# Optimization experiments

Hardware: AMD Instinct MI355X
Metric: run time of the kernel (lower is better)

## Reference

```python
import jax, jax.numpy as jnp
import numpy as np

N_NODES = 100000
N_EDGES = 1600000


def _gcn_conv(h, W, b, src, dst, n):
    """PyG GCNConv: linear, add self-loops, sym-normalized scatter-add, bias."""
    h = h @ W  # [n, out]
    # degree with self-loops: 1 (self loop) + in-degree over dst
    deg = jnp.ones((n,), dtype=h.dtype).at[dst].add(1.0)
    dinv = jax.lax.rsqrt(deg)  # deg >= 1, safe
    norm = dinv[src] * dinv[dst]  # [E]
    out = jnp.zeros_like(h).at[dst].add(norm[:, None] * h[src])
    out = out + (dinv * dinv)[:, None] * h  # self-loop contribution
    return out + b


def setup_inputs() -> dict:
    key = jax.random.key(0)
    ks = jax.random.split(key, 6)
    x = jax.random.normal(ks[0], (N_NODES, 5), dtype=jnp.float32)
    edge_index = jax.random.randint(ks[1], (2, N_EDGES), 0, N_NODES, dtype=jnp.int64)
    aff_w = jax.random.normal(ks[2], (3, 1), dtype=jnp.float32)
    cog_w = jax.random.normal(ks[3], (2, 1), dtype=jnp.float32)
    W1 = jax.random.normal(ks[4], (5, 64), dtype=jnp.float32) * 0.5
    b1 = jnp.zeros((64,), dtype=jnp.float32)
    W2 = jax.random.normal(ks[5], (64, 2), dtype=jnp.float32) * 0.125
    b2 = jnp.zeros((2,), dtype=jnp.float32)
    return {"x": x, "edge_index": edge_index, "aff_w": aff_w, "cog_w": cog_w,
            "W1": W1, "b1": b1, "W2": W2, "b2": b2}


def reference(x, edge_index, aff_w, cog_w, W1, b1, W2, b2):
    src, dst = edge_index[0], edge_index[1]
    n = x.shape[0]
    aff = x[:, :3]  # affective_indices = [0,1,2]
    cog = x[:, 3:5]  # cognitive_indices = [3,4]
    # attention: scores are [n,1]; softmax over dim=1 (size-1 axis), faithful to source
    s_a = jax.nn.softmax(aff @ aff_w, axis=1)
    s_c = jax.nn.softmax(cog @ cog_w, axis=1)
    h = jnp.concatenate([aff * s_a, cog * s_c], axis=1)  # [n,5]
    h = _gcn_conv(h, W1, b1, src, dst, n)
    h = jax.nn.relu(h)  # dropout is identity in eval mode
    h = _gcn_conv(h, W2, b2, src, dst, n)
    return jax.nn.log_softmax(h, axis=1)
```

## Files before the change

kernel.cpp:

```cpp
#include <hip/hip_runtime.h>


#define NPB     256
#define BSHIFT  8
#define BINCAP  6144
#define MAXBINS 512
#define ABLK    512
#define APT     8
#define BBLK    512
#define ROUNDS  3

__global__ __launch_bounds__(ABLK) void binA_k(const int* __restrict__ src, const int* __restrict__ dst,
                                               int E, int nbins, int* __restrict__ cursor,
                                               unsigned int* __restrict__ bpk) {
    __shared__ int hist[MAXBINS];
    __shared__ int gbase[MAXBINS];
    int t = threadIdx.x;
    hist[t] = 0;
    __syncthreads();
    int base = blockIdx.x * (ABLK * APT);
    int s_[APT], d_[APT], r_[APT];
#pragma unroll
    for (int r = 0; r < APT / 4; ++r) {
        int j0 = base + (r * ABLK + t) * 4;
        if (j0 + 3 < E) {
            int4 s4 = *(const int4*)(src + j0);
            int4 d4 = *(const int4*)(dst + j0);
            s_[r * 4 + 0] = s4.x; s_[r * 4 + 1] = s4.y; s_[r * 4 + 2] = s4.z; s_[r * 4 + 3] = s4.w;
            d_[r * 4 + 0] = d4.x; d_[r * 4 + 1] = d4.y; d_[r * 4 + 2] = d4.z; d_[r * 4 + 3] = d4.w;
#pragma unroll
            for (int q = 0; q < 4; ++q)
                r_[r * 4 + q] = atomicAdd(&hist[d_[r * 4 + q] >> BSHIFT], 1);
        } else {
#pragma unroll
            for (int q = 0; q < 4; ++q) {
                int e = j0 + q;
                if (e < E) {
                    s_[r * 4 + q] = src[e]; d_[r * 4 + q] = dst[e];
                    r_[r * 4 + q] = atomicAdd(&hist[d_[r * 4 + q] >> BSHIFT], 1);
                } else d_[r * 4 + q] = -1;
            }
        }
    }
    __syncthreads();
    if (t < nbins) {
        int h = hist[t];
        gbase[t] = h ? atomicAdd(&cursor[t], h) : 0;
    }
    __syncthreads();
#pragma unroll
    for (int q = 0; q < APT; ++q) {
        if (d_[q] >= 0) {
            int b = d_[q] >> BSHIFT;
            int pos = gbase[b] + r_[q];
            if (pos < BINCAP)
                bpk[(size_t)b * BINCAP + pos] = ((unsigned int)s_[q] << 8) | (unsigned int)(d_[q] & (NPB - 1));
        }
    }
}

__global__ __launch_bounds__(BBLK) void build_k(const int* __restrict__ cursor,
                                                const unsigned int* __restrict__ bpk,
                                                const float* __restrict__ x,
                                                int* __restrict__ sorted,
                                                int* __restrict__ row_start,
                                                unsigned short* __restrict__ row_cnt,
                                                float* __restrict__ dinv, float* __restrict__ y8, int n) {
    __shared__ int cnt[NPB];
    __shared__ int offs[NPB];
    __shared__ int srt[BINCAP];
    __shared__ int wsum[4];
    int b = blockIdx.x, t = threadIdx.x;
    if (t < NPB) cnt[t] = 0;
    __syncthreads();
    int m = cursor[b]; if (m > BINCAP) m = BINCAP;
    const unsigned int* pk = bpk + (size_t)b * BINCAP;

    unsigned int pv[ROUNDS][4];
    int rk[ROUNDS][4];
#pragma unroll
    for (int q = 0; q < ROUNDS; ++q) {
        int j0 = q * (BBLK * 4) + t * 4;
        if (j0 + 3 < m) {
            uint4 v = *(const uint4*)(pk + j0);
            pv[q][0] = v.x; pv[q][1] = v.y; pv[q][2] = v.z; pv[q][3] = v.w;
            rk[q][0] = atomicAdd(&cnt[v.x & 255u], 1);
            rk[q][1] = atomicAdd(&cnt[v.y & 255u], 1);
            rk[q][2] = atomicAdd(&cnt[v.z & 255u], 1);
            rk[q][3] = atomicAdd(&cnt[v.w & 255u], 1);
        } else {
#pragma unroll
            for (int qq = 0; qq < 4; ++qq) {
                int j = j0 + qq;
                if (j < m) { pv[q][qq] = pk[j]; rk[q][qq] = atomicAdd(&cnt[pv[q][qq] & 255u], 1); }
                else pv[q][qq] = 0xffffffffu;
            }
        }
    }
    __syncthreads();
    int c_ = 0, v = 0;
    int lane = t & 63, w = t >> 6;
    if (t < NPB) {
        c_ = cnt[t];
        v = c_;
#pragma unroll
        for (int dlt = 1; dlt < 64; dlt <<= 1) {
            int u = __shfl_up(v, dlt, 64);
            if (lane >= dlt) v += u;
        }
        if (lane == 63) wsum[w] = v;
    }
    __syncthreads();
    if (t < NPB) {
        int wo = 0;
#pragma unroll
        for (int k = 0; k < 4; ++k) if (k < w) wo += wsum[k];
        offs[t] = wo + v - c_;
    }
    __syncthreads();
#pragma unroll
    for (int q = 0; q < ROUNDS; ++q) {
#pragma unroll
        for (int qq = 0; qq < 4; ++qq) {
            unsigned int p = pv[q][qq];
            if (p != 0xffffffffu) {
                int j0 = q * (BBLK * 4) + t * 4 + qq;
                if (j0 < m) srt[offs[p & 255u] + rk[q][qq]] = (int)(p >> 8);
            }
        }
    }
    __syncthreads();
    int gb = b * BINCAP;
    for (int j0 = t * 4; j0 + 3 < m; j0 += BBLK * 4)
        *(int4*)(sorted + gb + j0) = *(const int4*)(srt + j0);
    if (t < 4) {
        int start = m & ~3;
        int j = start + t;
        if (j < m) sorted[gb + j] = srt[j];
    }
    int i = b * NPB + t;
    if (t < NPB && i < n) {
        row_start[i] = gb + offs[t];
        row_cnt[i] = (unsigned short)c_;
        float di = rsqrtf(1.0f + (float)c_);
        dinv[i] = di;
#pragma unroll
        for (int k = 0; k < 5; ++k) y8[(size_t)i * 8 + k] = di * x[i * 5 + k];
    }
}

__global__ __launch_bounds__(256) void gath1_mlp_k(const int* __restrict__ sorted,
                                                   const int* __restrict__ row_start,
                                                   const unsigned short* __restrict__ row_cnt,
                                                   const float* __restrict__ y8,
                                                   const float* __restrict__ dinv,
                                                   const float* __restrict__ W1, const float* __restrict__ b1,
                                                   const float* __restrict__ W2,
                                                   float* __restrict__ gy, int n) {
    __shared__ float W1s[320], b1s[64], W2s[128];
    int t = threadIdx.x;
    { int j = t; if (j < 320) W1s[j] = W1[j]; j = t + 256; if (j < 320) W1s[j] = W1[j]; }
    if (t < 64) b1s[t] = b1[t];
    if (t >= 64 && t < 192) W2s[t - 64] = W2[t - 64];
    __syncthreads();
    int grp = t >> 2, lane = t & 3;
    int i = blockIdx.x * 64 + grp;
    if (i >= n) return;
    int st = row_start[i];
    int e  = st + row_cnt[i];
    float a0 = 0.f, a1 = 0.f, a2 = 0.f, a3 = 0.f, a4 = 0.f;
    for (int j = st + lane; j < e; j += 4) {
        int s = sorted[j];
        float4 A = *(const float4*)(y8 + (size_t)s * 8);
        a0 += A.x; a1 += A.y; a2 += A.z; a3 += A.w;
        a4 += y8[(size_t)s * 8 + 4];
    }
    a0 += __shfl_xor(a0, 1); a0 += __shfl_xor(a0, 2);
    a1 += __shfl_xor(a1, 1); a1 += __shfl_xor(a1, 2);
    a2 += __shfl_xor(a2, 1); a2 += __shfl_xor(a2, 2);
    a3 += __shfl_xor(a3, 1); a3 += __shfl_xor(a3, 2);
    a4 += __shfl_xor(a4, 1); a4 += __shfl_xor(a4, 2);
    float4 S = *(const float4*)(y8 + (size_t)i * 8);
    float s4 = y8[(size_t)i * 8 + 4];
    float di = dinv[i];
    float v0 = di * (a0 + S.x);
    float v1 = di * (a1 + S.y);
    float v2 = di * (a2 + S.z);
    float v3 = di * (a3 + S.w);
    float v4 = di * (a4 + s4);
    float g0 = 0.f, g1 = 0.f;
#pragma unroll
    for (int q = 0; q < 16; ++q) {
        int jj = lane + q * 4;
        float h = b1s[jj];
        h = fmaf(v0, W1s[0 * 64 + jj], h);
        h = fmaf(v1, W1s[1 * 64 + jj], h);
        h = fmaf(v2, W1s[2 * 64 + jj], h);
        h = fmaf(v3, W1s[3 * 64 + jj], h);
        h = fmaf(v4, W1s[4 * 64 + jj], h);
        h = fmaxf(h, 0.f);
        g0 = fmaf(h, W2s[2 * jj], g0);
        g1 = fmaf(h, W2s[2 * jj + 1], g1);
    }
    g0 += __shfl_xor(g0, 1); g0 += __shfl_xor(g0, 2);
    g1 += __shfl_xor(g1, 1); g1 += __shfl_xor(g1, 2);
    if (lane == 0) {
        gy[i * 2] = di * g0; gy[i * 2 + 1] = di * g1;
    }
}

__global__ __launch_bounds__(256) void gath2_final_k(const int* __restrict__ sorted,
                                                     const int* __restrict__ row_start,
                                                     const unsigned short* __restrict__ row_cnt,
                                                     const float* __restrict__ gy,
                                                     const float* __restrict__ dinv,
                                                     const float* __restrict__ b2,
                                                     float* __restrict__ out, int n) {
    int t = threadIdx.x;
    int grp = t >> 2, lane = t & 3;
    int i = blockIdx.x * 64 + grp;
    if (i >= n) return;
    int st = row_start[i];
    int e  = st + row_cnt[i];
    float t0 = 0.f, t1 = 0.f;
    for (int j = st + lane; j < e; j += 4) {
        int s = sorted[j];
        float2 v = *(const float2*)(gy + (size_t)s * 2);
        t0 += v.x; t1 += v.y;
    }
    t0 += __shfl_xor(t0, 1); t0 += __shfl_xor(t0, 2);
    t1 += __shfl_xor(t1, 1); t1 += __shfl_xor(t1, 2);
    if (lane == 0) {
        float2 Sg = *(const float2*)(gy + (size_t)i * 2);
        float di = dinv[i];
        float o0 = di * (t0 + Sg.x) + b2[0];
        float o1 = di * (t1 + Sg.y) + b2[1];
        float mx = fmaxf(o0, o1);
        float lse = mx + logf(expf(o0 - mx) + expf(o1 - mx));
        out[i * 2]     = o0 - lse;
        out[i * 2 + 1] = o1 - lse;
    }
}

#define CAP 48
__global__ void fill_k(const int* __restrict__ src, const int* __restrict__ dst,
                       int E, int n, int* __restrict__ cnt, int* __restrict__ bucket) {
    int e = blockIdx.x * blockDim.x + threadIdx.x;
    if (e >= E) return;
    int s = src[e], d = dst[e];
    int slot = atomicAdd(&cnt[d], 1);
    if (slot < CAP) bucket[slot * n + d] = s;
}
__global__ void dinv_y_k(const float* __restrict__ x, const int* __restrict__ cnt,
                         float* __restrict__ dinv, float* __restrict__ y, int n) {
    int i = blockIdx.x * blockDim.x + threadIdx.x;
    if (i >= n) return;
    float di = rsqrtf(1.0f + (float)cnt[i]);
    dinv[i] = di;
#pragma unroll
    for (int k = 0; k < 5; ++k) y[i * 5 + k] = di * x[i * 5 + k];
}
__global__ void gather1_mlp_k(const float* __restrict__ x, const float* __restrict__ y,
                              const float* __restrict__ dinv, const int* __restrict__ cnt,
                              const int* __restrict__ bucket, int n,
                              const float* __restrict__ W1, const float* __restrict__ b1,
                              const float* __restrict__ W2,
                              float* __restrict__ g, float* __restrict__ gy) {
    __shared__ float W1s[320]; __shared__ float b1s[64]; __shared__ float W2s[128];
    int t = threadIdx.x;
    for (int j = t; j < 320; j += blockDim.x) W1s[j] = W1[j];
    if (t < 64) { b1s[t] = b1[t]; W2s[2 * t] = W2[2 * t]; W2s[2 * t + 1] = W2[2 * t + 1]; }
    __syncthreads();
    int i = blockIdx.x * blockDim.x + t;
    if (i >= n) return;
    int c = cnt[i]; if (c > CAP) c = CAP;
    float a0 = 0, a1 = 0, a2 = 0, a3 = 0, a4 = 0;
    for (int j = 0; j < c; ++j) {
        int s = bucket[j * n + i];
        const float* ys = y + s * 5;
        a0 += ys[0]; a1 += ys[1]; a2 += ys[2]; a3 += ys[3]; a4 += ys[4];
    }
    float di = dinv[i], d2 = di * di;
    float v0 = di * a0 + d2 * x[i * 5 + 0], v1 = di * a1 + d2 * x[i * 5 + 1];
    float v2 = di * a2 + d2 * x[i * 5 + 2], v3 = di * a3 + d2 * x[i * 5 + 3];
    float v4 = di * a4 + d2 * x[i * 5 + 4];
    float g0 = 0.f, g1 = 0.f;
#pragma unroll
    for (int j = 0; j < 64; ++j) {
        float h = b1s[j];
        h = fmaf(v0, W1s[j], h); h = fmaf(v1, W1s[64 + j], h); h = fmaf(v2, W1s[128 + j], h);
        h = fmaf(v3, W1s[192 + j], h); h = fmaf(v4, W1s[256 + j], h);
        h = fmaxf(h, 0.f);
        g0 = fmaf(h, W2s[2 * j], g0); g1 = fmaf(h, W2s[2 * j + 1], g1);
    }
    g[i * 2] = g0; g[i * 2 + 1] = g1;
    gy[i * 2] = di * g0; gy[i * 2 + 1] = di * g1;
}
__global__ void gather2_final_fb_k(const float* __restrict__ g, const float* __restrict__ gy,
                                   const float* __restrict__ dinv, const int* __restrict__ cnt,
                                   const int* __restrict__ bucket, int n,
                                   const float* __restrict__ b2, float* __restrict__ out) {
    int i = blockIdx.x * blockDim.x + threadIdx.x;
    if (i >= n) return;
    int c = cnt[i]; if (c > CAP) c = CAP;
    float t0 = 0.f, t1 = 0.f;
    for (int j = 0; j < c; ++j) {
        int s = bucket[j * n + i];
        t0 += gy[s * 2]; t1 += gy[s * 2 + 1];
    }
    float di = dinv[i], d2 = di * di;
    float o0 = di * t0 + d2 * g[i * 2] + b2[0];
    float o1 = di * t1 + d2 * g[i * 2 + 1] + b2[1];
    float mx = fmaxf(o0, o1);
    float lse = mx + logf(expf(o0 - mx) + expf(o1 - mx));
    out[i * 2] = o0 - lse; out[i * 2 + 1] = o1 - lse;
}

extern "C" void kernel_launch(void* const* d_in, const int* in_sizes, int n_in,
                              void* d_out, int out_size, void* d_ws, size_t ws_size,
                              hipStream_t stream) {
    const float* x  = (const float*)d_in[0];
    const int*   ei = (const int*)d_in[1];
    const float* W1 = (const float*)d_in[4];
    const float* b1 = (const float*)d_in[5];
    const float* W2 = (const float*)d_in[6];
    const float* b2 = (const float*)d_in[7];
    float* out = (float*)d_out;

    const int n = in_sizes[0] / 5;
    const int E = in_sizes[1] / 2;
    const int* src = ei;
    const int* dst = ei + E;

    const int nbins = (n + NPB - 1) >> BSHIFT;
    size_t need = (size_t)MAXBINS * 4 + (size_t)nbins * BINCAP * 8 +
                  (size_t)n * (4 + 2 + 4 + 32 + 8) + 64;

    if (nbins <= MAXBINS && n < (1 << 24) && ws_size >= need) {
        int* cursor = (int*)d_ws;
        unsigned int* bpk = (unsigned int*)(cursor + MAXBINS);
        int* sorted = (int*)(bpk + (size_t)nbins * BINCAP);
        int* row_start = sorted + (size_t)nbins * BINCAP;
        unsigned short* row_cnt = (unsigned short*)(row_start + n);
        float* dinv = (float*)(row_cnt + ((n + 1) & ~1));
        float* y8 = dinv + n;
        float* gy = y8 + 8 * (size_t)n;

        hipMemsetAsync(cursor, 0, MAXBINS * sizeof(int), stream);
        int ablocks = (E + ABLK * APT - 1) / (ABLK * APT);
        binA_k<<<ablocks, ABLK, 0, stream>>>(src, dst, E, nbins, cursor, bpk);
        build_k<<<nbins, BBLK, 0, stream>>>(cursor, bpk, x, sorted, row_start, row_cnt, dinv, y8, n);
        int g64 = (n + 63) / 64;
        gath1_mlp_k<<<g64, 256, 0, stream>>>(sorted, row_start, row_cnt, y8, dinv, W1, b1, W2, gy, n);
        gath2_final_k<<<g64, 256, 0, stream>>>(sorted, row_start, row_cnt, gy, dinv, b2, out, n);
    } else {
        const int BLK = 256;
        const int ngrid = (n + BLK - 1) / BLK;
        const int egrid = (E + BLK - 1) / BLK;
        int*   cnt    = (int*)d_ws;
        int*   bucket = cnt + n;
        float* dinv   = (float*)(bucket + (size_t)CAP * n);
        float* y      = dinv + n;
        float* g      = y + 5 * (size_t)n;
        float* gy     = g + 2 * (size_t)n;
        hipMemsetAsync(cnt, 0, (size_t)n * sizeof(int), stream);
        fill_k<<<egrid, BLK, 0, stream>>>(src, dst, E, n, cnt, bucket);
        dinv_y_k<<<ngrid, BLK, 0, stream>>>(x, cnt, dinv, y, n);
        gather1_mlp_k<<<ngrid, BLK, 0, stream>>>(x, y, dinv, cnt, bucket, n, W1, b1, W2, g, gy);
        gather2_final_fb_k<<<ngrid, BLK, 0, stream>>>(g, gy, dinv, cnt, bucket, n, b2, out);
    }
}
```

Measured before the change: 66.30 us.

## Stage binned edges in LDS for coalesced writes; widen gather groups to 8 lanes

The binning kernel now prefix-scans its per-bin histogram and places packed edges into a locally sorted shared-memory buffer. It then writes them out contiguously per bin, so global writes are coalesced instead of scattered. The two gather kernels now use 8 lanes per node instead of 4, with one more shuffle-reduction step, and the y8 buffer is aligned to 64 bytes. The cost is more shared memory and extra barriers in the binning kernel, plus half as many nodes per gather block.

```diff
diff --git a/kernel.cpp b/kernel.cpp
--- a/kernel.cpp
+++ b/kernel.cpp
@@ -7,6 +7,7 @@
 #define MAXBINS 512
 #define ABLK    512
 #define APT     8
+#define CHUNK   (ABLK * APT)
 #define BBLK    512
 #define ROUNDS  3
 
@@ -14,11 +15,15 @@
                                                int E, int nbins, int* __restrict__ cursor,
                                                unsigned int* __restrict__ bpk) {
     __shared__ int hist[MAXBINS];
+    __shared__ int lofs[MAXBINS];
     __shared__ int gbase[MAXBINS];
+    __shared__ int wsum8[8];
+    __shared__ unsigned int lpk[CHUNK];
+    __shared__ unsigned short lbin[CHUNK];
     int t = threadIdx.x;
     hist[t] = 0;
     __syncthreads();
-    int base = blockIdx.x * (ABLK * APT);
+    int base = blockIdx.x * CHUNK;
     int s_[APT], d_[APT], r_[APT];
 #pragma unroll
     for (int r = 0; r < APT / 4; ++r) {
@@ -43,19 +48,38 @@
         }
     }
     __syncthreads();
-    if (t < nbins) {
-        int h = hist[t];
-        gbase[t] = h ? atomicAdd(&cursor[t], h) : 0;
-    }
+    int c = hist[t];
+    gbase[t] = c ? atomicAdd(&cursor[t], c) : 0;
+    int lane = t & 63, w = t >> 6;
+    int v = c;
+#pragma unroll
+    for (int dlt = 1; dlt < 64; dlt <<= 1) {
+        int u = __shfl_up(v, dlt, 64);
+        if (lane >= dlt) v += u;
+    }
+    if (lane == 63) wsum8[w] = v;
+    __syncthreads();
+    int wo = 0;
+#pragma unroll
+    for (int k = 0; k < 8; ++k) if (k < w) wo += wsum8[k];
+    lofs[t] = wo + v - c;
     __syncthreads();
 #pragma unroll
     for (int q = 0; q < APT; ++q) {
         if (d_[q] >= 0) {
             int b = d_[q] >> BSHIFT;
-            int pos = gbase[b] + r_[q];
-            if (pos < BINCAP)
-                bpk[(size_t)b * BINCAP + pos] = ((unsigned int)s_[q] << 8) | (unsigned int)(d_[q] & (NPB - 1));
-        }
+            int idx = lofs[b] + r_[q];
+            lpk[idx]  = ((unsigned int)s_[q] << 8) | (unsigned int)(d_[q] & (NPB - 1));
+            lbin[idx] = (unsigned short)b;
+        }
+    }
+    __syncthreads();
+    int mblk = E - base; if (mblk > CHUNK) mblk = CHUNK;
+    for (int j = t; j < mblk; j += ABLK) {
+        unsigned int pk = lpk[j];
+        int b = lbin[j];
+        int gpos = gbase[b] + (j - lofs[b]);
+        if (gpos < BINCAP) bpk[(size_t)b * BINCAP + gpos] = pk;
     }
 }
 
@@ -163,23 +187,23 @@
     if (t < 64) b1s[t] = b1[t];
     if (t >= 64 && t < 192) W2s[t - 64] = W2[t - 64];
     __syncthreads();
-    int grp = t >> 2, lane = t & 3;
-    int i = blockIdx.x * 64 + grp;
+    int grp = t >> 3, lane = t & 7;
+    int i = blockIdx.x * 32 + grp;
     if (i >= n) return;
     int st = row_start[i];
     int e  = st + row_cnt[i];
     float a0 = 0.f, a1 = 0.f, a2 = 0.f, a3 = 0.f, a4 = 0.f;
-    for (int j = st + lane; j < e; j += 4) {
+    for (int j = st + lane; j < e; j += 8) {
         int s = sorted[j];
         float4 A = *(const float4*)(y8 + (size_t)s * 8);
         a0 += A.x; a1 += A.y; a2 += A.z; a3 += A.w;
         a4 += y8[(size_t)s * 8 + 4];
     }
-    a0 += __shfl_xor(a0, 1); a0 += __shfl_xor(a0, 2);
-    a1 += __shfl_xor(a1, 1); a1 += __shfl_xor(a1, 2);
-    a2 += __shfl_xor(a2, 1); a2 += __shfl_xor(a2, 2);
-    a3 += __shfl_xor(a3, 1); a3 += __shfl_xor(a3, 2);
-    a4 += __shfl_xor(a4, 1); a4 += __shfl_xor(a4, 2);
+    a0 += __shfl_xor(a0, 1); a0 += __shfl_xor(a0, 2); a0 += __shfl_xor(a0, 4);
+    a1 += __shfl_xor(a1, 1); a1 += __shfl_xor(a1, 2); a1 += __shfl_xor(a1, 4);
+    a2 += __shfl_xor(a2, 1); a2 += __shfl_xor(a2, 2); a2 += __shfl_xor(a2, 4);
+    a3 += __shfl_xor(a3, 1); a3 += __shfl_xor(a3, 2); a3 += __shfl_xor(a3, 4);
+    a4 += __shfl_xor(a4, 1); a4 += __shfl_xor(a4, 2); a4 += __shfl_xor(a4, 4);
     float4 S = *(const float4*)(y8 + (size_t)i * 8);
     float s4 = y8[(size_t)i * 8 + 4];
     float di = dinv[i];
@@ -190,8 +214,8 @@
     float v4 = di * (a4 + s4);
     float g0 = 0.f, g1 = 0.f;
 #pragma unroll
-    for (int q = 0; q < 16; ++q) {
-        int jj = lane + q * 4;
+    for (int q = 0; q < 8; ++q) {
+        int jj = lane + q * 8;
         float h = b1s[jj];
         h = fmaf(v0, W1s[0 * 64 + jj], h);
         h = fmaf(v1, W1s[1 * 64 + jj], h);
@@ -202,8 +226,8 @@
         g0 = fmaf(h, W2s[2 * jj], g0);
         g1 = fmaf(h, W2s[2 * jj + 1], g1);
     }
-    g0 += __shfl_xor(g0, 1); g0 += __shfl_xor(g0, 2);
-    g1 += __shfl_xor(g1, 1); g1 += __shfl_xor(g1, 2);
+    g0 += __shfl_xor(g0, 1); g0 += __shfl_xor(g0, 2); g0 += __shfl_xor(g0, 4);
+    g1 += __shfl_xor(g1, 1); g1 += __shfl_xor(g1, 2); g1 += __shfl_xor(g1, 4);
     if (lane == 0) {
         gy[i * 2] = di * g0; gy[i * 2 + 1] = di * g1;
     }
@@ -217,19 +241,19 @@
                                                      const float* __restrict__ b2,
                                                      float* __restrict__ out, int n) {
     int t = threadIdx.x;
-    int grp = t >> 2, lane = t & 3;
-    int i = blockIdx.x * 64 + grp;
+    int grp = t >> 3, lane = t & 7;
+    int i = blockIdx.x * 32 + grp;
     if (i >= n) return;
     int st = row_start[i];
     int e  = st + row_cnt[i];
     float t0 = 0.f, t1 = 0.f;
-    for (int j = st + lane; j < e; j += 4) {
+    for (int j = st + lane; j < e; j += 8) {
         int s = sorted[j];
         float2 v = *(const float2*)(gy + (size_t)s * 2);
         t0 += v.x; t1 += v.y;
     }
-    t0 += __shfl_xor(t0, 1); t0 += __shfl_xor(t0, 2);
-    t1 += __shfl_xor(t1, 1); t1 += __shfl_xor(t1, 2);
+    t0 += __shfl_xor(t0, 1); t0 += __shfl_xor(t0, 2); t0 += __shfl_xor(t0, 4);
+    t1 += __shfl_xor(t1, 1); t1 += __shfl_xor(t1, 2); t1 += __shfl_xor(t1, 4);
     if (lane == 0) {
         float2 Sg = *(const float2*)(gy + (size_t)i * 2);
         float di = dinv[i];
@@ -334,7 +358,7 @@
 
     const int nbins = (n + NPB - 1) >> BSHIFT;
     size_t need = (size_t)MAXBINS * 4 + (size_t)nbins * BINCAP * 8 +
-                  (size_t)n * (4 + 2 + 4 + 32 + 8) + 64;
+                  (size_t)n * (4 + 2 + 4 + 32 + 8) + 128;
 
     if (nbins <= MAXBINS && n < (1 << 24) && ws_size >= need) {
         int* cursor = (int*)d_ws;
@@ -343,16 +367,18 @@
         int* row_start = sorted + (size_t)nbins * BINCAP;
         unsigned short* row_cnt = (unsigned short*)(row_start + n);
         float* dinv = (float*)(row_cnt + ((n + 1) & ~1));
-        float* y8 = dinv + n;
+        uintptr_t yp = (uintptr_t)(dinv + n);
+        yp = (yp + 63) & ~(uintptr_t)63;
+        float* y8 = (float*)yp;
         float* gy = y8 + 8 * (size_t)n;
 
         hipMemsetAsync(cursor, 0, MAXBINS * sizeof(int), stream);
-        int ablocks = (E + ABLK * APT - 1) / (ABLK * APT);
+        int ablocks = (E + CHUNK - 1) / CHUNK;
         binA_k<<<ablocks, ABLK, 0, stream>>>(src, dst, E, nbins, cursor, bpk);
         build_k<<<nbins, BBLK, 0, stream>>>(cursor, bpk, x, sorted, row_start, row_cnt, dinv, y8, n);
-        int g64 = (n + 63) / 64;
-        gath1_mlp_k<<<g64, 256, 0, stream>>>(sorted, row_start, row_cnt, y8, dinv, W1, b1, W2, gy, n);
-        gath2_final_k<<<g64, 256, 0, stream>>>(sorted, row_start, row_cnt, gy, dinv, b2, out, n);
+        int g32 = (n + 31) / 32;
+        gath1_mlp_k<<<g32, 256, 0, stream>>>(sorted, row_start, row_cnt, y8, dinv, W1, b1, W2, gy, n);
+        gath2_final_k<<<g32, 256, 0, stream>>>(sorted, row_start, row_cnt, gy, dinv, b2, out, n);
     } else {
         const int BLK = 256;
         const int ngrid = (n + BLK - 1) / BLK;
```

After: 62.98 us. -5.0%, faster.
